# Kernel tuning notes

Measured on AMD Instinct MI355X. Metric: run time of the kernel, lower is better.

The kernel has to match this reference:

```python
import jax, jax.numpy as jnp
import numpy as np

K_RATIO = 0.2
EPS = 1e-6


def setup_inputs() -> dict:
    key = jax.random.key(0)
    k1, k2 = jax.random.split(key)
    B, C, D, H, W = 2, 4, 128, 128, 128
    logits = jax.random.normal(k1, (B, C, D, H, W), dtype=jnp.float32)
    labels = jax.random.randint(k2, (B, D, H, W), 0, C)
    # one-hot target along channel axis 1, matching the tensor-path `target` arg
    target = jax.nn.one_hot(labels, C, axis=1, dtype=jnp.float32)
    return {"logits": logits, "target": target}


def reference(logits, target):
    B, C = logits.shape[0], logits.shape[1]

    # ---- Top-K cross entropy (ignore_index=-1 -> all voxels valid) ----
    y = jnp.argmax(target, axis=1)  # [B, D, H, W] int labels
    logp = jax.nn.log_softmax(logits, axis=1)
    # CE per voxel: -logp[b, y, d, h, w]
    ce = -jnp.take_along_axis(logp, y[:, None], axis=1)[:, 0]  # [B, D, H, W]
    ce_flat = ce.reshape(B, -1)  # [B, N]
    N = ce_flat.shape[1]
    k = max(1, int(N * K_RATIO))  # static: all voxels valid, k < N
    topk_vals, _ = jax.lax.top_k(ce_flat, k)  # [B, k]
    topk_loss = jnp.mean(jnp.mean(topk_vals, axis=1))

    # ---- Soft dice (no valid_mask in tensor path) ----
    p = jax.nn.softmax(logits, axis=1)  # [B, C, D, H, W]
    spatial = tuple(range(2, p.ndim))
    num = 2.0 * jnp.sum(p * target, axis=spatial)          # [B, C]
    den = jnp.sum(p + target, axis=spatial) + EPS          # [B, C]
    dice = 1.0 - num / den                                  # [B, C]
    if C > 1:
        dice = dice[:, 1:]  # drop background channel
    dice_loss = jnp.mean(dice)

    return topk_loss + 0.5 * dice_loss
```

## Files before the change

kernel.cpp:

```cpp
#include <hip/hip_runtime.h>
#include <stdint.h>

#define NVOX (1u << 21)
#define NB   2
#define KSEL 419430u
#define TPB  256
#define VPB  4096
#define BPB  ((int)(NVOX / VPB))
#define NBLK (NB * BPB)
#define NBINS 2048
#define SH   20
#define FIXS 262144.0f

typedef unsigned long long u64;

__device__ __forceinline__ float wred64(float v) {
#pragma unroll
  for (int o = 32; o > 0; o >>= 1) v += __shfl_down(v, o, 64);
  return v;
}

__global__ __launch_bounds__(TPB, 4) void k1_fused(
    const float* __restrict__ logits, const float* __restrict__ target,
    u64* __restrict__ hist ,
    float* __restrict__ dice )
{
  __shared__ u64 hbin[NBINS];
  __shared__ float dsh[4][12];
  const int tid = threadIdx.x;
  for (int i = tid; i < NBINS; i += TPB) hbin[i] = 0ull;
  __syncthreads();

  const int blk = blockIdx.x;
  const int b = blk / BPB;
  const size_t v0 = (size_t)(blk % BPB) * VPB;
  const float* lg = logits + (size_t)b * 4 * NVOX + v0;
  const float* tg = target + (size_t)b * 4 * NVOX + v0;

  float sp[4] = {0.f,0.f,0.f,0.f}, nm[4] = {0.f,0.f,0.f,0.f}, ct[4] = {0.f,0.f,0.f,0.f};

#pragma unroll 2
  for (int i = tid * 4; i < VPB; i += TPB * 4) {
    float4 L[4], T[4];
#pragma unroll
    for (int c = 0; c < 4; ++c) {
      L[c] = *(const float4*)(lg + (size_t)c * NVOX + i);
      T[c] = *(const float4*)(tg + (size_t)c * NVOX + i);
    }
#pragma unroll
    for (int j = 0; j < 4; ++j) {
      float l[4], t[4];
#pragma unroll
      for (int c = 0; c < 4; ++c) {
        l[c] = ((const float*)&L[c])[j];
        t[c] = ((const float*)&T[c])[j];
      }
      float m = fmaxf(fmaxf(l[0], l[1]), fmaxf(l[2], l[3]));
      float e[4]; float s = 0.f;
#pragma unroll
      for (int c = 0; c < 4; ++c) { e[c] = __expf(l[c] - m); s += e[c]; }
      float inv = 1.f / s;
      float lse = __logf(s);
      float ly = l[0]*t[0] + l[1]*t[1] + l[2]*t[2] + l[3]*t[3];
      float cev = (m - ly) + lse;
      uint32_t idx = __float_as_uint(cev) >> SH;
      idx = min(idx, (uint32_t)(NBINS - 1));
      u64 pk = (1ull << 40) | (u64)(cev * FIXS);
      atomicAdd(&hbin[idx], pk);
#pragma unroll
      for (int c = 0; c < 4; ++c) {
        float p = e[c] * inv;
        sp[c] += p;
        nm[c] += p * t[c];
        ct[c] += t[c];
      }
    }
  }

#pragma unroll
  for (int c = 0; c < 4; ++c) { sp[c] = wred64(sp[c]); nm[c] = wred64(nm[c]); ct[c] = wred64(ct[c]); }
  if ((tid & 63) == 0) {
    const int w = tid >> 6;
#pragma unroll
    for (int c = 0; c < 4; ++c) {
      dsh[w][c]     = sp[c];
      dsh[w][4 + c] = nm[c];
      dsh[w][8 + c] = ct[c];
    }
  }
  __syncthreads();
  if (tid < 12)
    dice[(size_t)blk * 12 + tid] = dsh[0][tid] + dsh[1][tid] + dsh[2][tid] + dsh[3][tid];

  u64* hdst = hist + (size_t)blk * NBINS;
  for (int i = tid; i < NBINS; i += TPB) hdst[i] = hbin[i];
}

__global__ __launch_bounds__(256) void k_reduce(
    const u64* __restrict__ hist, uint32_t* __restrict__ rcnt,
    float* __restrict__ rsum)
{
  const int e = blockIdx.x;
  const int b = e >> 5;
  const int seg = e & 31;
  const int lane = threadIdx.x & 63;
  const int wave = threadIdx.x >> 6;
  const int bin = seg * 64 + lane;
  const u64* base = hist + (size_t)b * BPB * NBINS + bin;
  u64 csum = 0, fsum = 0;
  const int r0 = wave * (BPB / 4), r1 = r0 + BPB / 4;
  for (int r = r0; r < r1; ++r) {
    u64 v = base[(size_t)r * NBINS];
    csum += v >> 40;
    fsum += v & 0xFFFFFFFFFFull;
  }
  __shared__ u64 sc[4][64], ss[4][64];
  sc[wave][lane] = csum; ss[wave][lane] = fsum;
  __syncthreads();
  if (wave == 0) {
    csum = sc[0][lane] + sc[1][lane] + sc[2][lane] + sc[3][lane];
    fsum = ss[0][lane] + ss[1][lane] + ss[2][lane] + ss[3][lane];
    rcnt[b * NBINS + bin] = (uint32_t)csum;
    rsum[b * NBINS + bin] = (float)((double)fsum * (1.0 / 262144.0));
  }
}

__global__ __launch_bounds__(256) void k_final(
    const uint32_t* __restrict__ rcnt, const float* __restrict__ rsum,
    const float* __restrict__ dice, float* __restrict__ out)
{
  __shared__ uint32_t shc[NBINS];
  __shared__ uint32_t chunk[256];
  __shared__ uint32_t sbkt, srem;
  __shared__ float wpart[4];
  __shared__ float ts[NB];
  __shared__ float cpart[4][24];
  const int tid = threadIdx.x;

  for (int b = 0; b < NB; ++b) {
    const uint32_t* rc = rcnt + (size_t)b * NBINS;
    const float*    rs = rsum + (size_t)b * NBINS;
    uint32_t s = 0;
#pragma unroll
    for (int q = 0; q < 2; ++q) {
      uint4 v = *(const uint4*)(rc + tid * 8 + q * 4);
      *(uint4*)&shc[tid * 8 + q * 4] = v;
      s += v.x + v.y + v.z + v.w;
    }
    chunk[tid] = s;
    __syncthreads();
    if (tid == 0) {
      uint32_t k = KSEL, cum = 0;
      int ci = 255;
      for (; ci > 0; --ci) {
        uint32_t c = chunk[ci];
        if (cum + c >= k) break;
        cum += c;
      }
      int bkt = ci * 8;
      for (int j = 7; j >= 0; --j) {
        uint32_t c = shc[ci * 8 + j];
        if (cum + c >= k) { bkt = ci * 8 + j; break; }
        cum += c;
      }
      sbkt = (uint32_t)bkt;
      srem = k - cum;
    }
    __syncthreads();
    const int bkt = (int)sbkt;
    float w = 0.f;
#pragma unroll
    for (int j = 0; j < 8; ++j) {
      int bin = tid * 8 + j;
      if (bin > bkt) w += rs[bin];
    }
    w = wred64(w);
    if ((tid & 63) == 0) wpart[tid >> 6] = w;
    __syncthreads();
    if (tid == 0) {
      float cnt_t = (float)shc[bkt];
      float sum_t = rs[bkt];
      float lo = __uint_as_float((uint32_t)bkt << SH);
      float hi = __uint_as_float((uint32_t)(bkt + 1) << SH);
      float width = hi - lo;
      float avg = sum_t / cnt_t;
      float frac = (float)srem / cnt_t;
      float est = avg + (1.f - frac) * 0.5f * width;
      ts[b] = wpart[0] + wpart[1] + wpart[2] + wpart[3] + (float)srem * est;
    }
    __syncthreads();
  }

  float a0[12], a1[12];
#pragma unroll
  for (int c = 0; c < 12; ++c) { a0[c] = 0.f; a1[c] = 0.f; }
  for (int r = tid; r < NBLK; r += 256) {
    const float* dp = dice + (size_t)r * 12;
    if (r < BPB) {
#pragma unroll
      for (int c = 0; c < 12; ++c) a0[c] += dp[c];
    } else {
#pragma unroll
      for (int c = 0; c < 12; ++c) a1[c] += dp[c];
    }
  }
#pragma unroll
  for (int c = 0; c < 12; ++c) { a0[c] = wred64(a0[c]); a1[c] = wred64(a1[c]); }
  if ((tid & 63) == 0) {
    const int w = tid >> 6;
#pragma unroll
    for (int c = 0; c < 12; ++c) { cpart[w][c] = a0[c]; cpart[w][12 + c] = a1[c]; }
  }
  __syncthreads();
  if (tid == 0) {
    float comp[24];
#pragma unroll
    for (int c = 0; c < 24; ++c)
      comp[c] = cpart[0][c] + cpart[1][c] + cpart[2][c] + cpart[3][c];
    float dl = 0.f;
#pragma unroll
    for (int b = 0; b < 2; ++b)
#pragma unroll
      for (int c = 1; c < 4; ++c) {
        float sp = comp[b * 12 + c];
        float nm = comp[b * 12 + 4 + c];
        float ct = comp[b * 12 + 8 + c];
        dl += 1.f - (2.f * nm) / (sp + ct + 1e-6f);
      }
    float topk = 0.5f * (ts[0] + ts[1]) / (float)KSEL;
    out[0] = topk + 0.5f * (dl / 6.f);
  }
}

extern "C" void kernel_launch(void* const* d_in, const int* in_sizes, int n_in,
                              void* d_out, int out_size, void* d_ws, size_t ws_size,
                              hipStream_t stream) {
  (void)in_sizes; (void)n_in; (void)out_size; (void)ws_size;
  const float* logits = (const float*)d_in[0];
  const float* target = (const float*)d_in[1];
  float* out = (float*)d_out;

  char* ws = (char*)d_ws;
  u64*      hist = (u64*)ws;
  float*    dice = (float*)(hist + (size_t)NBLK * NBINS);
  uint32_t* rcnt = (uint32_t*)(dice + (size_t)NBLK * 12);
  float*    rsum = (float*)(rcnt + (size_t)NB * NBINS);

  k1_fused<<<NBLK, TPB, 0, stream>>>(logits, target, hist, dice);
  k_reduce<<<64, 256, 0, stream>>>(hist, rcnt, rsum);
  k_final<<<1, 256, 0, stream>>>(rcnt, rsum, dice, out);
}
```

Measured before the change: 179.9 us.

## Split CE/dice pass from histogram using 16-bit CE codes and windowed bins

The fused kernel no longer does per-voxel shared-memory u64 atomics into a 2048-bin histogram. It also no longer writes a full per-block histogram to global memory. Instead it stores a 16-bit truncated float code of each voxel's CE value. A separate kernel reads those codes and builds a 256-bin histogram over a fixed exponent window. This shrinks histogram traffic and the reduce/final passes, at the cost of an extra 8MB code write/read, coarser CE values, and dropping values outside the window. The change also halves voxels per block and uses a hardware reciprocal for the softmax normalisation.

```diff
diff --git a/kernel.cpp b/kernel.cpp
--- a/kernel.cpp
+++ b/kernel.cpp
@@ -5,11 +5,13 @@
 #define NB   2
 #define KSEL 419430u
 #define TPB  256
-#define VPB  4096
+#define VPB  2048
 #define BPB  ((int)(NVOX / VPB))
-#define NBLK (NB * BPB)
-#define NBINS 2048
-#define SH   20
+#define ABLK (NB * BPB)
+#define BBLK 1024
+#define CPBB 4096
+#define WLO  960u
+#define WN   256
 #define FIXS 262144.0f
 
 typedef unsigned long long u64;
@@ -20,26 +22,23 @@
   return v;
 }
 
-__global__ __launch_bounds__(TPB, 4) void k1_fused(
+__global__ __launch_bounds__(TPB, 4) void kA_ce_dice(
     const float* __restrict__ logits, const float* __restrict__ target,
-    u64* __restrict__ hist ,
+    uint16_t* __restrict__ codes ,
     float* __restrict__ dice )
 {
-  __shared__ u64 hbin[NBINS];
   __shared__ float dsh[4][12];
   const int tid = threadIdx.x;
-  for (int i = tid; i < NBINS; i += TPB) hbin[i] = 0ull;
-  __syncthreads();
-
   const int blk = blockIdx.x;
   const int b = blk / BPB;
   const size_t v0 = (size_t)(blk % BPB) * VPB;
   const float* lg = logits + (size_t)b * 4 * NVOX + v0;
   const float* tg = target + (size_t)b * 4 * NVOX + v0;
+  uint16_t* cb = codes + (size_t)b * NVOX + v0;
 
   float sp[4] = {0.f,0.f,0.f,0.f}, nm[4] = {0.f,0.f,0.f,0.f}, ct[4] = {0.f,0.f,0.f,0.f};
 
-#pragma unroll 2
+#pragma unroll
   for (int i = tid * 4; i < VPB; i += TPB * 4) {
     float4 L[4], T[4];
 #pragma unroll
@@ -47,6 +46,8 @@
       L[c] = *(const float4*)(lg + (size_t)c * NVOX + i);
       T[c] = *(const float4*)(tg + (size_t)c * NVOX + i);
     }
+    ushort4 out;
+    uint16_t* op = (uint16_t*)&out;
 #pragma unroll
     for (int j = 0; j < 4; ++j) {
       float l[4], t[4];
@@ -59,14 +60,11 @@
       float e[4]; float s = 0.f;
 #pragma unroll
       for (int c = 0; c < 4; ++c) { e[c] = __expf(l[c] - m); s += e[c]; }
-      float inv = 1.f / s;
+      float inv = __builtin_amdgcn_rcpf(s);
       float lse = __logf(s);
       float ly = l[0]*t[0] + l[1]*t[1] + l[2]*t[2] + l[3]*t[3];
       float cev = (m - ly) + lse;
-      uint32_t idx = __float_as_uint(cev) >> SH;
-      idx = min(idx, (uint32_t)(NBINS - 1));
-      u64 pk = (1ull << 40) | (u64)(cev * FIXS);
-      atomicAdd(&hbin[idx], pk);
+      op[j] = (uint16_t)(__float_as_uint(cev) >> 15);
 #pragma unroll
       for (int c = 0; c < 4; ++c) {
         float p = e[c] * inv;
@@ -75,6 +73,7 @@
         ct[c] += t[c];
       }
     }
+    *(ushort4*)(cb + i) = out;
   }
 
 #pragma unroll
@@ -91,9 +90,41 @@
   __syncthreads();
   if (tid < 12)
     dice[(size_t)blk * 12 + tid] = dsh[0][tid] + dsh[1][tid] + dsh[2][tid] + dsh[3][tid];
-
-  u64* hdst = hist + (size_t)blk * NBINS;
-  for (int i = tid; i < NBINS; i += TPB) hdst[i] = hbin[i];
+}
+
+__global__ __launch_bounds__(TPB, 4) void kB_hist(
+    const uint16_t* __restrict__ codes,
+    u64* __restrict__ hist )
+{
+  __shared__ u64 hb[WN];
+  const int tid = threadIdx.x;
+  if (tid < WN) hb[tid] = 0ull;
+  __syncthreads();
+
+  const int bc = blockIdx.x;
+  const size_t base = (size_t)bc * CPBB;
+  const uint4* p = (const uint4*)(codes + base);
+
+#pragma unroll
+  for (int it = 0; it < CPBB / (TPB * 8); ++it) {
+    uint4 v = p[it * TPB + tid];
+    const uint32_t ws[4] = {v.x, v.y, v.z, v.w};
+#pragma unroll
+    for (int q = 0; q < 4; ++q) {
+#pragma unroll
+      for (int h = 0; h < 2; ++h) {
+        uint32_t c = (h == 0) ? (ws[q] & 0xFFFFu) : (ws[q] >> 16);
+        uint32_t idx = (c >> 5) - WLO;
+        if (idx < WN) {
+          float dec = __uint_as_float((c << 15) | 0x4000u);
+          u64 pk = (1ull << 40) | (u64)(dec * FIXS);
+          atomicAdd(&hb[idx], pk);
+        }
+      }
+    }
+  }
+  __syncthreads();
+  if (tid < WN) hist[(size_t)bc * WN + tid] = hb[tid];
 }
 
 __global__ __launch_bounds__(256) void k_reduce(
@@ -101,16 +132,16 @@
     float* __restrict__ rsum)
 {
   const int e = blockIdx.x;
-  const int b = e >> 5;
-  const int seg = e & 31;
+  const int b = e >> 2;
+  const int seg = e & 3;
   const int lane = threadIdx.x & 63;
   const int wave = threadIdx.x >> 6;
   const int bin = seg * 64 + lane;
-  const u64* base = hist + (size_t)b * BPB * NBINS + bin;
+  const int rows = BBLK / NB;
   u64 csum = 0, fsum = 0;
-  const int r0 = wave * (BPB / 4), r1 = r0 + BPB / 4;
+  const int r0 = wave * (rows / 4), r1 = r0 + rows / 4;
   for (int r = r0; r < r1; ++r) {
-    u64 v = base[(size_t)r * NBINS];
+    u64 v = hist[(size_t)(b * rows + r) * WN + bin];
     csum += v >> 40;
     fsum += v & 0xFFFFFFFFFFull;
   }
@@ -120,8 +151,8 @@
   if (wave == 0) {
     csum = sc[0][lane] + sc[1][lane] + sc[2][lane] + sc[3][lane];
     fsum = ss[0][lane] + ss[1][lane] + ss[2][lane] + ss[3][lane];
-    rcnt[b * NBINS + bin] = (uint32_t)csum;
-    rsum[b * NBINS + bin] = (float)((double)fsum * (1.0 / 262144.0));
+    rcnt[b * WN + bin] = (uint32_t)csum;
+    rsum[b * WN + bin] = (float)((double)fsum * (1.0 / 262144.0));
   }
 }
 
@@ -129,8 +160,7 @@
     const uint32_t* __restrict__ rcnt, const float* __restrict__ rsum,
     const float* __restrict__ dice, float* __restrict__ out)
 {
-  __shared__ uint32_t shc[NBINS];
-  __shared__ uint32_t chunk[256];
+  __shared__ uint32_t shc[WN];
   __shared__ uint32_t sbkt, srem;
   __shared__ float wpart[4];
   __shared__ float ts[NB];
@@ -138,50 +168,32 @@
   const int tid = threadIdx.x;
 
   for (int b = 0; b < NB; ++b) {
-    const uint32_t* rc = rcnt + (size_t)b * NBINS;
-    const float*    rs = rsum + (size_t)b * NBINS;
-    uint32_t s = 0;
-#pragma unroll
-    for (int q = 0; q < 2; ++q) {
-      uint4 v = *(const uint4*)(rc + tid * 8 + q * 4);
-      *(uint4*)&shc[tid * 8 + q * 4] = v;
-      s += v.x + v.y + v.z + v.w;
-    }
-    chunk[tid] = s;
+    const uint32_t cnt = rcnt[b * WN + tid];
+    const float    sm  = rsum[b * WN + tid];
+    shc[tid] = cnt;
     __syncthreads();
     if (tid == 0) {
-      uint32_t k = KSEL, cum = 0;
-      int ci = 255;
-      for (; ci > 0; --ci) {
-        uint32_t c = chunk[ci];
-        if (cum + c >= k) break;
+      uint32_t k = KSEL, cum = 0, rem = 1;
+      int bkt = 0;
+      for (int i = WN - 1; i >= 0; --i) {
+        uint32_t c = shc[i];
+        if (cum + c >= k) { bkt = i; rem = k - cum; break; }
         cum += c;
       }
-      int bkt = ci * 8;
-      for (int j = 7; j >= 0; --j) {
-        uint32_t c = shc[ci * 8 + j];
-        if (cum + c >= k) { bkt = ci * 8 + j; break; }
-        cum += c;
-      }
       sbkt = (uint32_t)bkt;
-      srem = k - cum;
+      srem = rem;
     }
     __syncthreads();
     const int bkt = (int)sbkt;
-    float w = 0.f;
-#pragma unroll
-    for (int j = 0; j < 8; ++j) {
-      int bin = tid * 8 + j;
-      if (bin > bkt) w += rs[bin];
-    }
+    float w = (tid > bkt) ? sm : 0.f;
     w = wred64(w);
     if ((tid & 63) == 0) wpart[tid >> 6] = w;
     __syncthreads();
     if (tid == 0) {
       float cnt_t = (float)shc[bkt];
-      float sum_t = rs[bkt];
-      float lo = __uint_as_float((uint32_t)bkt << SH);
-      float hi = __uint_as_float((uint32_t)(bkt + 1) << SH);
+      float sum_t = rsum[b * WN + bkt];
+      float lo = __uint_as_float((WLO + (uint32_t)bkt) << 20);
+      float hi = __uint_as_float((WLO + (uint32_t)bkt + 1) << 20);
       float width = hi - lo;
       float avg = sum_t / cnt_t;
       float frac = (float)srem / cnt_t;
@@ -194,7 +206,7 @@
   float a0[12], a1[12];
 #pragma unroll
   for (int c = 0; c < 12; ++c) { a0[c] = 0.f; a1[c] = 0.f; }
-  for (int r = tid; r < NBLK; r += 256) {
+  for (int r = tid; r < ABLK; r += 256) {
     const float* dp = dice + (size_t)r * 12;
     if (r < BPB) {
 #pragma unroll
@@ -241,12 +253,14 @@
   float* out = (float*)d_out;
 
   char* ws = (char*)d_ws;
-  u64*      hist = (u64*)ws;
-  float*    dice = (float*)(hist + (size_t)NBLK * NBINS);
-  uint32_t* rcnt = (uint32_t*)(dice + (size_t)NBLK * 12);
-  float*    rsum = (float*)(rcnt + (size_t)NB * NBINS);
-
-  k1_fused<<<NBLK, TPB, 0, stream>>>(logits, target, hist, dice);
-  k_reduce<<<64, 256, 0, stream>>>(hist, rcnt, rsum);
+  u64*      hist  = (u64*)ws;
+  uint16_t* codes = (uint16_t*)(hist + (size_t)BBLK * WN);
+  float*    dice  = (float*)(codes + (size_t)NB * NVOX);
+  uint32_t* rcnt  = (uint32_t*)(dice + (size_t)ABLK * 12);
+  float*    rsum  = (float*)(rcnt + NB * WN);
+
+  kA_ce_dice<<<ABLK, TPB, 0, stream>>>(logits, target, codes, dice);
+  kB_hist<<<BBLK, TPB, 0, stream>>>(codes, hist);
+  k_reduce<<<8, 256, 0, stream>>>(hist, rcnt, rsum);
   k_final<<<1, 256, 0, stream>>>(rcnt, rsum, dice, out);
 }
```

New measurement: 186.3 us. 1.04x slower.
